# Optimization experiments

Measured on AMD Instinct MI355X. Metric: run time of the kernel, lower is better.

## Reference

```python
import jax, jax.numpy as jnp
import numpy as np

EPS = 1e-12  # torch F.normalize eps


def _pairwise_unit_diffs(x):
    # x: [B, N, D] -> unit-normalized pairwise diffs [B, N*N, D]
    B, N, D = x.shape
    d = x[:, :, None, :] - x[:, None, :, :]            # [B, N, N, D]
    n = jnp.linalg.norm(d, axis=-1, keepdims=True)
    d = d / jnp.maximum(n, EPS)                        # zero rows stay zero
    return d.reshape(B, N * N, D)


def setup_inputs() -> dict:
    key = jax.random.key(0)
    k1, k2 = jax.random.split(key)
    B, N, D = 4, 64, 128
    student = jax.random.normal(k1, (B, N, D), dtype=jnp.float32)
    teacher = jax.random.normal(k2, (B, N, D), dtype=jnp.float32)
    return {"student": student, "teacher": teacher}


def reference(student, teacher):
    B, N, D = student.shape
    sd = _pairwise_unit_diffs(student)                              # [B, N^2, D]
    td = jax.lax.stop_gradient(_pairwise_unit_diffs(teacher))      # [B, N^2, D]
    s_ang = jnp.einsum('bkd,bld->bkl', sd, sd)
    t_ang = jax.lax.stop_gradient(jnp.einsum('bkd,bld->bkl', td, td))
    # smooth L1 (beta=1.0), summed then divided by total element count
    diff = s_ang - t_ang
    ad = jnp.abs(diff)
    loss = jnp.where(ad < 1.0, 0.5 * diff * diff, ad - 0.5)
    count = B * (N * N) * (N * N)
    return jnp.sum(loss) / count
```

## Files before the change

### kernel.cpp

```cpp
#include <hip/hip_runtime.h>


#define EPSQ 1e-24f

typedef __bf16 bf16x8 __attribute__((ext_vector_type(8)));
typedef float  f32x4  __attribute__((ext_vector_type(4)));

__device__ __forceinline__ float rinv_nsq(float nsq)
{
    return __builtin_amdgcn_rsqf(fmaxf(nsq, EPSQ));
}

__device__ __forceinline__ void cvt8(float4 u, float4 v, bf16x8& h, bf16x8& l)
{
    float uu[8] = {u.x, u.y, u.z, u.w, v.x, v.y, v.z, v.w};
#pragma unroll
    for (int i = 0; i < 8; ++i) {
        __bf16 hh = (__bf16)uu[i];
        h[i] = hh;
        l[i] = (__bf16)(uu[i] - (float)hh);
    }
}

__global__ __launch_bounds__(1024) void fused_kernel(
    const float* __restrict__ student, const float* __restrict__ teacher,
    float* __restrict__ out)
{
    __shared__ float Gs[4096];
    __shared__ float Gt[4096];
    __shared__ __align__(16) float pool[17408];
    __shared__ float red[16];

    int b   = blockIdx.x / 63;
    int kc  = blockIdx.x % 63;
    int tid = threadIdx.x;

    {
        int r = tid >> 4;
        int h = tid & 15;
        const float* Xs = student + b * 8192 + r * 128 + h * 8;
        const float* Xt = teacher + b * 8192 + r * 128 + h * 8;
        float* sHi = pool + 0 * 4352 + r * 68 + h * 4;
        float* sLo = pool + 1 * 4352 + r * 68 + h * 4;
        float* tHi = pool + 2 * 4352 + r * 68 + h * 4;
        float* tLo = pool + 3 * 4352 + r * 68 + h * 4;
        float4 u = *(const float4*)(Xs);
        float4 v = *(const float4*)(Xs + 4);
        bf16x8 hh, ll;
        cvt8(u, v, hh, ll);
        *(bf16x8*)sHi = hh;
        *(bf16x8*)sLo = ll;
        u = *(const float4*)(Xt);
        v = *(const float4*)(Xt + 4);
        cvt8(u, v, hh, ll);
        *(bf16x8*)tHi = hh;
        *(bf16x8*)tLo = ll;
    }
    __syncthreads();

    {
        int wid  = tid >> 6;
        int lane = tid & 63;
        int l15  = lane & 15;
        int quad = lane >> 4;
        int tensor = wid >> 3;
        int w8     = wid & 7;
        int mt     = w8 >> 1;
        int nh     = w8 & 1;
        const float* XH = pool + tensor * 8704;
        const float* XL = XH + 4352;

        bf16x8 aH[4], aL[4];
        int abase = (mt * 16 + l15) * 68 + quad * 4;
#pragma unroll
        for (int ks = 0; ks < 4; ++ks) {
            aH[ks] = *(const bf16x8*)(XH + abase + ks * 16);
            aL[ks] = *(const bf16x8*)(XL + abase + ks * 16);
        }
        float* Gd = tensor ? Gt : Gs;
#pragma unroll
        for (int nn = 0; nn < 2; ++nn) {
            int nt = nh * 2 + nn;
            f32x4 acc = {0.f, 0.f, 0.f, 0.f};
            int bbase = (nt * 16 + l15) * 68 + quad * 4;
#pragma unroll
            for (int ks = 0; ks < 4; ++ks) {
                bf16x8 bH = *(const bf16x8*)(XH + bbase + ks * 16);
                bf16x8 bL = *(const bf16x8*)(XL + bbase + ks * 16);
                acc = __builtin_amdgcn_mfma_f32_16x16x32_bf16(aH[ks], bH, acc, 0, 0, 0);
                acc = __builtin_amdgcn_mfma_f32_16x16x32_bf16(aH[ks], bL, acc, 0, 0, 0);
                acc = __builtin_amdgcn_mfma_f32_16x16x32_bf16(aL[ks], bH, acc, 0, 0, 0);
                acc = __builtin_amdgcn_mfma_f32_16x16x32_bf16(aL[ks], bL, acc, 0, 0, 0);
            }
#pragma unroll
            for (int reg = 0; reg < 4; ++reg)
                Gd[(mt * 16 + quad * 4 + reg) * 64 + nt * 16 + l15] = acc[reg];
        }
    }
    __syncthreads();

    float* vs  = pool;
    float* vt  = pool + 2176;
    float* rnS = pool + 4352;
    float* rnT = pool + 8448;

    {
        int tensor = tid >> 9;
        int u      = tid & 511;
        int p      = u >> 3;
        int q0     = (u & 7) * 8;
        const float* Gd = tensor ? Gt : Gs;
        float*       rn = tensor ? rnT : rnS;
        float dp = Gd[p * 65];
        float4 g0 = *(const float4*)(Gd + p * 64 + q0);
        float4 g1 = *(const float4*)(Gd + p * 64 + q0 + 4);
        float4 o0, o1;
        o0.x = rinv_nsq(dp - 2.f * g0.x + Gd[(q0 + 0) * 65]);
        o0.y = rinv_nsq(dp - 2.f * g0.y + Gd[(q0 + 1) * 65]);
        o0.z = rinv_nsq(dp - 2.f * g0.z + Gd[(q0 + 2) * 65]);
        o0.w = rinv_nsq(dp - 2.f * g0.w + Gd[(q0 + 3) * 65]);
        o1.x = rinv_nsq(dp - 2.f * g1.x + Gd[(q0 + 4) * 65]);
        o1.y = rinv_nsq(dp - 2.f * g1.y + Gd[(q0 + 5) * 65]);
        o1.z = rinv_nsq(dp - 2.f * g1.z + Gd[(q0 + 6) * 65]);
        o1.w = rinv_nsq(dp - 2.f * g1.w + Gd[(q0 + 7) * 65]);
        *(float4*)(rn + p * 64 + q0)     = o0;
        *(float4*)(rn + p * 64 + q0 + 4) = o1;
    }
    __syncthreads();

    {
        int m  = tid >> 5;
        int qh = (tid & 31) * 2;
        int t  = kc * 32 + m;
        int i = (int)(0.5f * (127.0f - sqrtf((float)(16129 - 8 * t))));
        if (i * (127 - i) / 2 > t) --i;
        else if ((i + 1) * (126 - i) / 2 <= t) ++i;
        int j = i + 1 + (t - i * (127 - i) / 2);

        float rsij = rnS[i * 64 + j];
        float rtij = rnT[i * 64 + j];

        float2 gi = *(const float2*)(Gs + i * 64 + qh);
        float2 gj = *(const float2*)(Gs + j * 64 + qh);
        float2 o;
        o.x = (gi.x - gj.x) * rsij;
        o.y = (gi.y - gj.y) * rsij;
        *(float2*)(vs + m * 68 + qh) = o;
        gi = *(const float2*)(Gt + i * 64 + qh);
        gj = *(const float2*)(Gt + j * 64 + qh);
        o.x = (gi.x - gj.x) * rtij;
        o.y = (gi.y - gj.y) * rtij;
        *(float2*)(vt + m * 68 + qh) = o;
    }

    int msub = tid >> 7;
    int pos  = tid & 127;
    int pg = 0, qg = 0;
    float4 rsv[4], rtv[4];
    if (pos < 120) {
        pg = (int)(0.5f * (31.0f - sqrtf((float)(961 - 8 * pos))));
        if (pg * (31 - pg) / 2 > pos) --pg;
        else if ((pg + 1) * (30 - pg) / 2 <= pos) ++pg;
        qg = pg + 1 + (pos - pg * (31 - pg) / 2);
        int p4 = pg * 4;
#pragma unroll
        for (int k = 0; k < 4; ++k) {
            rsv[k] = *(const float4*)(rnS + (qg * 4 + k) * 64 + p4);
            rtv[k] = *(const float4*)(rnT + (qg * 4 + k) * 64 + p4);
        }
    }
    __syncthreads();

    float ac0 = 0.f, ac1 = 0.f, ac2 = 0.f, ac3 = 0.f;

#define SL1(acc, spc, sqc, tpc, tqc, rsk, rtk)                                  \
    {                                                                           \
        float d  = (spc - sqc) * rsk - (tpc - tqc) * rtk;                       \
        float a  = fabsf(d);                                                    \
        float mn = fminf(a, 1.0f);                                              \
        acc = fmaf(mn, fmaf(-0.5f, mn, a), acc);                                \
    }

    if (pos < 120) {
        int p4  = pg * 4;
        int q4l = qg * 4;
#pragma unroll
        for (int mm = 0; mm < 4; ++mm) {
            int m = mm * 8 + msub;
            const float* vsm = vs + m * 68;
            const float* vtm = vt + m * 68;
            float4 sp = *(const float4*)(vsm + p4);
            float4 tp = *(const float4*)(vtm + p4);
            float4 sq = *(const float4*)(vsm + q4l);
            float4 tq = *(const float4*)(vtm + q4l);

            SL1(ac0, sp.x, sq.x, tp.x, tq.x, rsv[0].x, rtv[0].x)
            SL1(ac0, sp.y, sq.x, tp.y, tq.x, rsv[0].y, rtv[0].y)
            SL1(ac0, sp.z, sq.x, tp.z, tq.x, rsv[0].z, rtv[0].z)
            SL1(ac0, sp.w, sq.x, tp.w, tq.x, rsv[0].w, rtv[0].w)

            SL1(ac1, sp.x, sq.y, tp.x, tq.y, rsv[1].x, rtv[1].x)
            SL1(ac1, sp.y, sq.y, tp.y, tq.y, rsv[1].y, rtv[1].y)
            SL1(ac1, sp.z, sq.y, tp.z, tq.y, rsv[1].z, rtv[1].z)
            SL1(ac1, sp.w, sq.y, tp.w, tq.y, rsv[1].w, rtv[1].w)

            SL1(ac2, sp.x, sq.z, tp.x, tq.z, rsv[2].x, rtv[2].x)
            SL1(ac2, sp.y, sq.z, tp.y, tq.z, rsv[2].y, rtv[2].y)
            SL1(ac2, sp.z, sq.z, tp.z, tq.z, rsv[2].z, rtv[2].z)
            SL1(ac2, sp.w, sq.z, tp.w, tq.z, rsv[2].w, rtv[2].w)

            SL1(ac3, sp.x, sq.w, tp.x, tq.w, rsv[3].x, rtv[3].x)
            SL1(ac3, sp.y, sq.w, tp.y, tq.w, rsv[3].y, rtv[3].y)
            SL1(ac3, sp.z, sq.w, tp.z, tq.w, rsv[3].z, rtv[3].z)
            SL1(ac3, sp.w, sq.w, tp.w, tq.w, rsv[3].w, rtv[3].w)
        }
    }

    if (tid < 512) {
        int m  = tid >> 4;
        int g4 = (tid & 15) * 4;
        float4 s4 = *(const float4*)(vs + m * 68 + g4);
        float4 t4 = *(const float4*)(vt + m * 68 + g4);

        float rs01 = rnS[(g4 + 0) * 64 + g4 + 1];
        float rs02 = rnS[(g4 + 0) * 64 + g4 + 2];
        float rs03 = rnS[(g4 + 0) * 64 + g4 + 3];
        float rs12 = rnS[(g4 + 1) * 64 + g4 + 2];
        float rs13 = rnS[(g4 + 1) * 64 + g4 + 3];
        float rs23 = rnS[(g4 + 2) * 64 + g4 + 3];
        float rt01 = rnT[(g4 + 0) * 64 + g4 + 1];
        float rt02 = rnT[(g4 + 0) * 64 + g4 + 2];
        float rt03 = rnT[(g4 + 0) * 64 + g4 + 3];
        float rt12 = rnT[(g4 + 1) * 64 + g4 + 2];
        float rt13 = rnT[(g4 + 1) * 64 + g4 + 3];
        float rt23 = rnT[(g4 + 2) * 64 + g4 + 3];

        SL1(ac0, s4.x, s4.y, t4.x, t4.y, rs01, rt01)
        SL1(ac1, s4.x, s4.z, t4.x, t4.z, rs02, rt02)
        SL1(ac2, s4.x, s4.w, t4.x, t4.w, rs03, rt03)
        SL1(ac3, s4.y, s4.z, t4.y, t4.z, rs12, rt12)
        SL1(ac0, s4.y, s4.w, t4.y, t4.w, rs13, rt13)
        SL1(ac1, s4.z, s4.w, t4.z, t4.w, rs23, rt23)
    }
#undef SL1

    float acc = (ac0 + ac1) + (ac2 + ac3);

    for (int off = 32; off > 0; off >>= 1)
        acc += __shfl_down(acc, off);
    int lane = tid & 63;
    int wave = tid >> 6;
    if (lane == 0) red[wave] = acc;
    __syncthreads();
    if (tid < 16) {
        float v = red[tid];
        v += __shfl_down(v, 8);
        v += __shfl_down(v, 4);
        v += __shfl_down(v, 2);
        v += __shfl_down(v, 1);
        if (tid == 0) atomicAdd(out, v * (1.0f / 16777216.0f));
    }
}

extern "C" void kernel_launch(void* const* d_in, const int* in_sizes, int n_in,
                              void* d_out, int out_size, void* d_ws, size_t ws_size,
                              hipStream_t stream)
{
    const float* student = (const float*)d_in[0];
    const float* teacher = (const float*)d_in[1];
    (void)d_ws; (void)ws_size;
    fused_kernel<<<252, 1024, 0, stream>>>(student, teacher, (float*)d_out);
}
```

Baseline: 66.03 us.

## Drop low-low MFMA term, remove a barrier, and pack smooth-L1 math into float2

```diff
diff --git a/kernel.cpp b/kernel.cpp
--- a/kernel.cpp
+++ b/kernel.cpp
@@ -5,10 +5,18 @@
 
 typedef __bf16 bf16x8 __attribute__((ext_vector_type(8)));
 typedef float  f32x4  __attribute__((ext_vector_type(4)));
+typedef float  f32x2  __attribute__((ext_vector_type(2)));
 
 __device__ __forceinline__ float rinv_nsq(float nsq)
 {
     return __builtin_amdgcn_rsqf(fmaxf(nsq, EPSQ));
+}
+
+__device__ __forceinline__ float sl1a(float acc, float d)
+{
+    float a  = fabsf(d);
+    float mn = fminf(a, 1.0f);
+    return fmaf(mn, fmaf(-0.5f, mn, a), acc);
 }
 
 __device__ __forceinline__ void cvt8(float4 u, float4 v, bf16x8& h, bf16x8& l)
@@ -90,7 +98,6 @@
                 acc = __builtin_amdgcn_mfma_f32_16x16x32_bf16(aH[ks], bH, acc, 0, 0, 0);
                 acc = __builtin_amdgcn_mfma_f32_16x16x32_bf16(aH[ks], bL, acc, 0, 0, 0);
                 acc = __builtin_amdgcn_mfma_f32_16x16x32_bf16(aL[ks], bH, acc, 0, 0, 0);
-                acc = __builtin_amdgcn_mfma_f32_16x16x32_bf16(aL[ks], bL, acc, 0, 0, 0);
             }
 #pragma unroll
             for (int reg = 0; reg < 4; ++reg)
@@ -126,19 +133,18 @@
         *(float4*)(rn + p * 64 + q0)     = o0;
         *(float4*)(rn + p * 64 + q0 + 4) = o1;
     }
-    __syncthreads();
-
     {
         int m  = tid >> 5;
         int qh = (tid & 31) * 2;
         int t  = kc * 32 + m;
-        int i = (int)(0.5f * (127.0f - sqrtf((float)(16129 - 8 * t))));
+        float sq = __builtin_amdgcn_sqrtf((float)(16129 - 8 * t));
+        int i = (int)(0.5f * (127.0f - sq));
         if (i * (127 - i) / 2 > t) --i;
         else if ((i + 1) * (126 - i) / 2 <= t) ++i;
         int j = i + 1 + (t - i * (127 - i) / 2);
 
-        float rsij = rnS[i * 64 + j];
-        float rtij = rnT[i * 64 + j];
+        float rsij = rinv_nsq(Gs[i * 65] - 2.f * Gs[i * 64 + j] + Gs[j * 65]);
+        float rtij = rinv_nsq(Gt[i * 65] - 2.f * Gt[i * 64 + j] + Gt[j * 65]);
 
         float2 gi = *(const float2*)(Gs + i * 64 + qh);
         float2 gj = *(const float2*)(Gs + j * 64 + qh);
@@ -156,34 +162,31 @@
     int msub = tid >> 7;
     int pos  = tid & 127;
     int pg = 0, qg = 0;
-    float4 rsv[4], rtv[4];
     if (pos < 120) {
-        pg = (int)(0.5f * (31.0f - sqrtf((float)(961 - 8 * pos))));
+        float sq = __builtin_amdgcn_sqrtf((float)(961 - 8 * pos));
+        pg = (int)(0.5f * (31.0f - sq));
         if (pg * (31 - pg) / 2 > pos) --pg;
         else if ((pg + 1) * (30 - pg) / 2 <= pos) ++pg;
         qg = pg + 1 + (pos - pg * (31 - pg) / 2);
-        int p4 = pg * 4;
-#pragma unroll
-        for (int k = 0; k < 4; ++k) {
-            rsv[k] = *(const float4*)(rnS + (qg * 4 + k) * 64 + p4);
-            rtv[k] = *(const float4*)(rnT + (qg * 4 + k) * 64 + p4);
-        }
     }
     __syncthreads();
 
     float ac0 = 0.f, ac1 = 0.f, ac2 = 0.f, ac3 = 0.f;
-
-#define SL1(acc, spc, sqc, tpc, tqc, rsk, rtk)                                  \
-    {                                                                           \
-        float d  = (spc - sqc) * rsk - (tpc - tqc) * rtk;                       \
-        float a  = fabsf(d);                                                    \
-        float mn = fminf(a, 1.0f);                                              \
-        acc = fmaf(mn, fmaf(-0.5f, mn, a), acc);                                \
-    }
 
     if (pos < 120) {
         int p4  = pg * 4;
         int q4l = qg * 4;
+        f32x2 rsA[4], rsB[4], rtA[4], rtB[4];
+#pragma unroll
+        for (int k = 0; k < 4; ++k) {
+            float4 r = *(const float4*)(rnS + (qg * 4 + k) * 64 + p4);
+            rsA[k] = f32x2{r.x, r.y};
+            rsB[k] = f32x2{r.z, r.w};
+            r = *(const float4*)(rnT + (qg * 4 + k) * 64 + p4);
+            rtA[k] = f32x2{r.x, r.y};
+            rtB[k] = f32x2{r.z, r.w};
+        }
+
 #pragma unroll
         for (int mm = 0; mm < 4; ++mm) {
             int m = mm * 8 + msub;
@@ -193,26 +196,25 @@
             float4 tp = *(const float4*)(vtm + p4);
             float4 sq = *(const float4*)(vsm + q4l);
             float4 tq = *(const float4*)(vtm + q4l);
-
-            SL1(ac0, sp.x, sq.x, tp.x, tq.x, rsv[0].x, rtv[0].x)
-            SL1(ac0, sp.y, sq.x, tp.y, tq.x, rsv[0].y, rtv[0].y)
-            SL1(ac0, sp.z, sq.x, tp.z, tq.x, rsv[0].z, rtv[0].z)
-            SL1(ac0, sp.w, sq.x, tp.w, tq.x, rsv[0].w, rtv[0].w)
-
-            SL1(ac1, sp.x, sq.y, tp.x, tq.y, rsv[1].x, rtv[1].x)
-            SL1(ac1, sp.y, sq.y, tp.y, tq.y, rsv[1].y, rtv[1].y)
-            SL1(ac1, sp.z, sq.y, tp.z, tq.y, rsv[1].z, rtv[1].z)
-            SL1(ac1, sp.w, sq.y, tp.w, tq.y, rsv[1].w, rtv[1].w)
-
-            SL1(ac2, sp.x, sq.z, tp.x, tq.z, rsv[2].x, rtv[2].x)
-            SL1(ac2, sp.y, sq.z, tp.y, tq.z, rsv[2].y, rtv[2].y)
-            SL1(ac2, sp.z, sq.z, tp.z, tq.z, rsv[2].z, rtv[2].z)
-            SL1(ac2, sp.w, sq.z, tp.w, tq.z, rsv[2].w, rtv[2].w)
-
-            SL1(ac3, sp.x, sq.w, tp.x, tq.w, rsv[3].x, rtv[3].x)
-            SL1(ac3, sp.y, sq.w, tp.y, tq.w, rsv[3].y, rtv[3].y)
-            SL1(ac3, sp.z, sq.w, tp.z, tq.w, rsv[3].z, rtv[3].z)
-            SL1(ac3, sp.w, sq.w, tp.w, tq.w, rsv[3].w, rtv[3].w)
+            f32x2 spA = {sp.x, sp.y}, spB = {sp.z, sp.w};
+            f32x2 tpA = {tp.x, tp.y}, tpB = {tp.z, tp.w};
+
+#define COLK(acck, sqk, tqk, kk)                                          \
+            {                                                             \
+                f32x2 sqv = {sqk, sqk};                                   \
+                f32x2 tqv = {tqk, tqk};                                   \
+                f32x2 dA = (spA - sqv) * rsA[kk] - (tpA - tqv) * rtA[kk]; \
+                f32x2 dB = (spB - sqv) * rsB[kk] - (tpB - tqv) * rtB[kk]; \
+                acck = sl1a(acck, dA.x);                                  \
+                acck = sl1a(acck, dA.y);                                  \
+                acck = sl1a(acck, dB.x);                                  \
+                acck = sl1a(acck, dB.y);                                  \
+            }
+            COLK(ac0, sq.x, tq.x, 0)
+            COLK(ac1, sq.y, tq.y, 1)
+            COLK(ac2, sq.z, tq.z, 2)
+            COLK(ac3, sq.w, tq.w, 3)
+#undef COLK
         }
     }
 
@@ -235,14 +237,13 @@
         float rt13 = rnT[(g4 + 1) * 64 + g4 + 3];
         float rt23 = rnT[(g4 + 2) * 64 + g4 + 3];
 
-        SL1(ac0, s4.x, s4.y, t4.x, t4.y, rs01, rt01)
-        SL1(ac1, s4.x, s4.z, t4.x, t4.z, rs02, rt02)
-        SL1(ac2, s4.x, s4.w, t4.x, t4.w, rs03, rt03)
-        SL1(ac3, s4.y, s4.z, t4.y, t4.z, rs12, rt12)
-        SL1(ac0, s4.y, s4.w, t4.y, t4.w, rs13, rt13)
-        SL1(ac1, s4.z, s4.w, t4.z, t4.w, rs23, rt23)
-    }
-#undef SL1
+        ac0 = sl1a(ac0, (s4.x - s4.y) * rs01 - (t4.x - t4.y) * rt01);
+        ac1 = sl1a(ac1, (s4.x - s4.z) * rs02 - (t4.x - t4.z) * rt02);
+        ac2 = sl1a(ac2, (s4.x - s4.w) * rs03 - (t4.x - t4.w) * rt03);
+        ac3 = sl1a(ac3, (s4.y - s4.z) * rs12 - (t4.y - t4.z) * rt12);
+        ac0 = sl1a(ac0, (s4.y - s4.w) * rs13 - (t4.y - t4.w) * rt13);
+        ac1 = sl1a(ac1, (s4.z - s4.w) * rs23 - (t4.z - t4.w) * rt23);
+    }
 
     float acc = (ac0 + ac1) + (ac2 + ac3);
 
```

After: 65.61 us. No clear change (-0.6%).
